# Optimization experiments

Hardware: AMD Instinct MI355X
Metric: run time of the kernel (lower is better)

Reference implementation:

```python
import jax, jax.numpy as jnp
import numpy as np

NPOINT = 1024
RADIUS = 0.2
NSAMPLE = 64
BN_EPS = 1e-5


def setup_inputs() -> dict:
    key = jax.random.key(0)
    ks = jax.random.split(key, 16)
    B, N = 8, 8192
    inp = {
        "xyz": jax.random.normal(ks[0], (B, 3, N), jnp.float32),
        "points": jax.random.normal(ks[1], (B, 3, N), jnp.float32),
        "seed_inds": jax.random.randint(ks[2], (B, N), 0, N),
    }
    chans = [6, 64, 64, 128]
    for i in range(3):
        cin, cout = chans[i], chans[i + 1]
        kk = jax.random.split(ks[3 + i], 3)
        inp[f"w{i}"] = jax.random.normal(kk[0], (cout, cin), jnp.float32) / np.sqrt(cin)
        inp[f"b{i}"] = jnp.zeros((cout,), jnp.float32)
        inp[f"g{i}"] = jnp.ones((cout,), jnp.float32)
        inp[f"be{i}"] = jnp.zeros((cout,), jnp.float32)
        inp[f"m{i}"] = jax.random.normal(kk[1], (cout,), jnp.float32) * 0.1
        inp[f"v{i}"] = jax.random.uniform(kk[2], (cout,), jnp.float32, 0.5, 1.5)
    return inp


def _fps(xyz, npoint):
    # xyz: [B, N, 3]. Deterministic start at index 0 (torch uses a random start).
    B, N, _ = xyz.shape

    def step(carry, _):
        dist, far = carry
        cent = jnp.take_along_axis(xyz, far[:, None, None], axis=1)  # [B,1,3]
        d = jnp.sum((xyz - cent) ** 2, -1)                           # [B,N]
        dist = jnp.minimum(dist, d)
        nxt = jnp.argmax(dist, -1)
        return (dist, nxt), far

    init = (jnp.full((B, N), 1e10, xyz.dtype), jnp.zeros((B,), jnp.int32))
    _, idxs = jax.lax.scan(step, init, None, length=npoint)
    return idxs.T  # [B, npoint]


def _sqdist(src, dst):
    # src [B,S,3], dst [B,N,3] -> [B,S,N]
    d = -2.0 * jnp.einsum("bsc,bnc->bsn", src, dst)
    d += jnp.sum(src ** 2, -1)[:, :, None]
    d += jnp.sum(dst ** 2, -1)[:, None, :]
    return d


def _gather(pts, idx):
    # pts [B,N,C], idx [B,S,K] -> [B,S,K,C]
    B, S, K = idx.shape
    flat = jnp.take_along_axis(pts, idx.reshape(B, S * K, 1), axis=1)
    return flat.reshape(B, S, K, pts.shape[-1])


def _forward(xyz, points, seed_inds, layers):
    xyz_t = xyz.transpose(0, 2, 1)      # [B,N,3]
    pts_t = points.transpose(0, 2, 1)   # [B,N,D]
    B, N, _ = xyz_t.shape

    fps_idx = _fps(xyz_t, NPOINT)                                   # [B,S]
    new_seed = jnp.take_along_axis(seed_inds, fps_idx.astype(seed_inds.dtype), axis=1)
    new_xyz = jnp.take_along_axis(xyz_t, fps_idx[:, :, None], axis=1)  # [B,S,3]

    # ball query via sort trick (same math as torch module)
    sq = _sqdist(new_xyz, xyz_t)                                    # [B,S,N]
    gi = jnp.where(sq > RADIUS ** 2, N, jnp.arange(N, dtype=jnp.int32)[None, None, :])
    gi = jnp.sort(gi, axis=-1)[:, :, :NSAMPLE]                      # [B,S,K]
    first = gi[:, :, :1]
    gi = jnp.where(gi == N, first, gi)

    gxyz = _gather(xyz_t, gi) - new_xyz[:, :, None, :]              # [B,S,K,3]
    gpts = _gather(pts_t, gi)                                       # [B,S,K,D]
    feat = jnp.concatenate([gxyz, gpts], -1)                        # [B,S,K,3+D]

    for (w, b, g, be, m, v) in layers:
        feat = jnp.einsum("bskc,oc->bsko", feat, w) + b             # 1x1 conv
        feat = (feat - m) * (g / jnp.sqrt(v + BN_EPS)) + be         # BN (inference)
        feat = jax.nn.relu(feat)

    new_points = jnp.max(feat, axis=2).transpose(0, 2, 1)           # [B,Cout,S]
    return new_xyz.transpose(0, 2, 1), new_points, new_seed


def reference(xyz, points, seed_inds,
              w0, b0, g0, be0, m0, v0,
              w1, b1, g1, be1, m1, v1,
              w2, b2, g2, be2, m2, v2):
    layers = [(w0, b0, g0, be0, m0, v0),
              (w1, b1, g1, be1, m1, v1),
              (w2, b2, g2, be2, m2, v2)]
    return _forward(xyz, points, seed_inds, layers)
```

## Files before the change

### kernel.cpp

```cpp
#include <hip/hip_runtime.h>

#define B_ 8
#define N_ 8192
#define S_ 1024
#define NS_ 64

typedef float v2f __attribute__((ext_vector_type(2)));
typedef unsigned long long u64;
typedef short bf16x8 __attribute__((ext_vector_type(8)));
typedef float f32x4 __attribute__((ext_vector_type(4)));

#define OUT0 0
#define OUT1 24576
#define OUT2 1073152

template <int CTRL>
static __device__ __forceinline__ float dpp_max_step(float v) {
    int o = __builtin_amdgcn_update_dpp(__float_as_int(v), __float_as_int(v),
                                        CTRL, 0xf, 0xf, false);
    return fmaxf(v, __int_as_float(o));
}
static __device__ __forceinline__ float wave_max_f32(float v) {
    v = dpp_max_step<0x111>(v);
    v = dpp_max_step<0x112>(v);
    v = dpp_max_step<0x114>(v);
    v = dpp_max_step<0x118>(v);
    v = dpp_max_step<0x142>(v);
    v = dpp_max_step<0x143>(v);
    return __int_as_float(__builtin_amdgcn_readlane(__float_as_int(v), 63));
}
template <int CTRL>
static __device__ __forceinline__ unsigned dpp_umin_step(unsigned v) {
    unsigned o = (unsigned)__builtin_amdgcn_update_dpp((int)v, (int)v,
                                                       CTRL, 0xf, 0xf, false);
    return v < o ? v : o;
}
static __device__ __forceinline__ unsigned wave_min_u32(unsigned v) {
    v = dpp_umin_step<0x111>(v);
    v = dpp_umin_step<0x112>(v);
    v = dpp_umin_step<0x114>(v);
    v = dpp_umin_step<0x118>(v);
    v = dpp_umin_step<0x142>(v);
    v = dpp_umin_step<0x143>(v);
    return (unsigned)__builtin_amdgcn_readlane((int)v, 63);
}

static __device__ __forceinline__ short f2bf(float f) {
    unsigned u = __float_as_uint(f);
    return (short)((u + 0x7FFFu + ((u >> 16) & 1u)) >> 16);
}

#define FPS_T 256
#define FPS_J 16

__global__ __launch_bounds__(FPS_T, 1) void fps_kernel(const float* __restrict__ xyz,
                                                       float* out) {
    const int b = blockIdx.x;
    const int t = threadIdx.x;
    const int lane = t & 63;
    const int wq = t >> 6;
    const float* X = xyz + b * 3 * N_;

    v2f px2[FPS_J], py2[FPS_J], pz2[FPS_J], dist2[FPS_J];
#pragma unroll
    for (int j = 0; j < FPS_J; ++j) {
        int n = t + 512 * j;
        px2[j] = (v2f){X[n], X[n + 256]};
        py2[j] = (v2f){X[N_ + n], X[N_ + n + 256]};
        pz2[j] = (v2f){X[2 * N_ + n], X[2 * N_ + n + 256]};
        dist2[j] = (v2f){1e10f, 1e10f};
    }

    __shared__ u64 slots[8];
    float* oseed = out + OUT2 + b * S_;

    int ci = 0;
    float c0 = X[0], c1 = X[N_], c2 = X[2 * N_];

    for (int step = 0; step < S_; ++step) {
        if (t == 0) oseed[step] = __int_as_float(ci);

        v2f mv = (v2f){-1.0f, -1.0f};
        {
#pragma clang fp contract(off)
            v2f c0v = (v2f){c0, c0};
            v2f c1v = (v2f){c1, c1};
            v2f c2v = (v2f){c2, c2};
#pragma unroll
            for (int j = 0; j < FPS_J; ++j) {
                v2f e0 = px2[j] - c0v;
                v2f e1 = py2[j] - c1v;
                v2f e2 = pz2[j] - c2v;
                v2f q0 = e0 * e0;
                v2f q1 = e1 * e1;
                v2f q2 = e2 * e2;
                v2f d  = (q0 + q1) + q2;
                v2f dm = __builtin_elementwise_min(dist2[j], d);
                dist2[j] = dm;
                mv = __builtin_elementwise_max(mv, dm);
            }
        }
        float m = fmaxf(mv.x, mv.y);
        float wmax = wave_max_f32(m);

        unsigned mask = 0u;
#pragma unroll
        for (int j = 0; j < FPS_J; ++j) {
            if (dist2[j].x == wmax) mask |= (1u << (2 * j));
            if (dist2[j].y == wmax) mask |= (1u << (2 * j + 1));
        }
        unsigned cand = 0xffffffffu;
        if (mask) {
            unsigned c = (unsigned)(__ffs(mask) - 1);
            cand = (unsigned)t | (c << 8);
        }
        unsigned widx = wave_min_u32(cand);

        if (lane == 63) {
            u64 key = ((u64)__float_as_uint(wmax) << 13) | (u64)(8191u - widx);
            slots[((step & 1) << 2) + wq] = key;
        }
        __syncthreads();

        const u64* sp = &slots[(step & 1) << 2];
        u64 k0 = sp[0], k1 = sp[1], k2 = sp[2], k3 = sp[3];
        u64 ka = (k0 > k1) ? k0 : k1;
        u64 kb = (k2 > k3) ? k2 : k3;
        u64 km = (ka > kb) ? ka : kb;
        ci = 8191 - (int)(km & 0x1fffull);

        int cu = __builtin_amdgcn_readfirstlane(ci);
        c0 = X[cu];
        c1 = X[N_ + cu];
        c2 = X[2 * N_ + cu];
    }
}

__global__ __launch_bounds__(256) void wconv_kernel(const float* __restrict__ w1,
                                                    const float* __restrict__ w2,
                                                    short* __restrict__ wbf) {
    int t = blockIdx.x * 256 + threadIdx.x;
    float v = (t < 4096) ? w1[t] : w2[t - 4096];
    wbf[t] = f2bf(v);
}

__global__ __launch_bounds__(256) void down_kernel(
    const float* __restrict__ xyz, const float* __restrict__ pts,
    const int* __restrict__ seed,
    const float* __restrict__ w0, const float* __restrict__ b0,
    const float* __restrict__ g0, const float* __restrict__ be0,
    const float* __restrict__ m0, const float* __restrict__ v0,
    const float* __restrict__ w1, const float* __restrict__ b1,
    const float* __restrict__ g1, const float* __restrict__ be1,
    const float* __restrict__ m1, const float* __restrict__ v1,
    const float* __restrict__ w2, const float* __restrict__ b2,
    const float* __restrict__ g2, const float* __restrict__ be2,
    const float* __restrict__ m2, const float* __restrict__ v2,
    float* out, const short* __restrict__ wbf) {
    const int sg = blockIdx.x;
    const int b = sg >> 10, s = sg & 1023;
    const int t = threadIdx.x;
    const int lane = t & 63;
    const int wq = __builtin_amdgcn_readfirstlane(t >> 6);
    const int ln = lane & 15;
    const int quad = (lane >> 4) & 3;

    __shared__ float f0[64 * 9];
    __shared__ short featA[64 * 72];
    __shared__ short featB[64 * 72];
    __shared__ float wmaxs[4 * 132];
    __shared__ float scs[256], ofs[256];
    __shared__ int cand[4 * 64];
    __shared__ int cnts[4];
    __shared__ int gis[64];

    const float* X = xyz + b * 3 * N_;

    int ci = __float_as_int(out[OUT2 + sg]) & 8191;
    float cx = X[ci], cy = X[N_ + ci], cz = X[2 * N_ + ci];

    {
        float sc, of;
        if (t < 64) {
            int c = t;
            sc = g0[c] / sqrtf(v0[c] + 1e-5f);
            of = (b0[c] - m0[c]) * sc + be0[c];
        } else if (t < 128) {
            int c = t - 64;
            sc = g1[c] / sqrtf(v1[c] + 1e-5f);
            of = (b1[c] - m1[c]) * sc + be1[c];
        } else {
            int c = t - 128;
            sc = g2[c] / sqrtf(v2[c] + 1e-5f);
            of = (b2[c] - m2[c]) * sc + be2[c];
        }
        scs[t] = sc;
        ofs[t] = of;
    }
    __syncthreads();

    if (t == 0) {
        out[OUT0 + (b * 3 + 0) * S_ + s] = cx;
        out[OUT0 + (b * 3 + 1) * S_ + s] = cy;
        out[OUT0 + (b * 3 + 2) * S_ + s] = cz;
        out[OUT2 + sg] = (float)seed[b * N_ + ci];
    }

    {
        int cnt = 0;
        const int wbase = wq << 11;
#pragma unroll 2
        for (int base = 0; base < 2048; base += 128) {
            int n0 = wbase + base + lane;
            int n1 = n0 + 64;
            float x0 = X[n0], y0 = X[N_ + n0], z0 = X[2 * N_ + n0];
            float x1 = X[n1], y1 = X[N_ + n1], z1 = X[2 * N_ + n1];
            float e0 = x0 - cx, e1 = y0 - cy, e2 = z0 - cz;
            float d0 = fmaf(e2, e2, fmaf(e1, e1, e0 * e0));
            float q0 = x1 - cx, q1 = y1 - cy, q2 = z1 - cz;
            float d1 = fmaf(q2, q2, fmaf(q1, q1, q0 * q0));

            u64 mask0 = __ballot(d0 <= 0.04f);
            if (mask0) {
                int pos = cnt + (int)__popcll(mask0 & ((1ull << lane) - 1ull));
                if ((d0 <= 0.04f) && pos < NS_) cand[(wq << 6) + pos] = n0;
                cnt += (int)__popcll(mask0);
            }
            u64 mask1 = __ballot(d1 <= 0.04f);
            if (mask1) {
                int pos = cnt + (int)__popcll(mask1 & ((1ull << lane) - 1ull));
                if ((d1 <= 0.04f) && pos < NS_) cand[(wq << 6) + pos] = n1;
                cnt += (int)__popcll(mask1);
            }
        }
        if (lane == 0) cnts[wq] = cnt;
    }
    __syncthreads();

    if (t < 64) {
        int k = t;
        int start = 0, sel = -1, firstv = -1;
#pragma unroll
        for (int w = 0; w < 4; ++w) {
            int cw = min(cnts[w], NS_);
            if (firstv < 0 && cw > 0) firstv = cand[(w << 6)];
            if (sel < 0 && k < start + cw) sel = cand[(w << 6) + (k - start)];
            start += cw;
        }
        if (sel < 0) sel = firstv;
        gis[t] = sel;
    }
    __syncthreads();

    if (t < 64) {
        int gidx = gis[t] & 8191;
        const float* P = pts + b * 3 * N_;
        f0[t * 9 + 0] = X[gidx] - cx;
        f0[t * 9 + 1] = X[N_ + gidx] - cy;
        f0[t * 9 + 2] = X[2 * N_ + gidx] - cz;
        f0[t * 9 + 3] = P[gidx];
        f0[t * 9 + 4] = P[N_ + gidx];
        f0[t * 9 + 5] = P[2 * N_ + gidx];
    }
    __syncthreads();

    {
        float in[6];
#pragma unroll
        for (int c = 0; c < 6; ++c) in[c] = f0[lane * 9 + c];
#pragma unroll 1
        for (int i = 0; i < 16; i += 4) {
            int o = wq * 16 + i;
            float a0 = 0.f, a1 = 0.f, a2 = 0.f, a3 = 0.f;
#pragma unroll
            for (int c = 0; c < 6; ++c) {
                float rc = in[c];
                a0 = fmaf(rc, w0[(o + 0) * 6 + c], a0);
                a1 = fmaf(rc, w0[(o + 1) * 6 + c], a1);
                a2 = fmaf(rc, w0[(o + 2) * 6 + c], a2);
                a3 = fmaf(rc, w0[(o + 3) * 6 + c], a3);
            }
            featA[lane * 72 + o + 0] = f2bf(fmaxf(fmaf(a0, scs[o + 0], ofs[o + 0]), 0.f));
            featA[lane * 72 + o + 1] = f2bf(fmaxf(fmaf(a1, scs[o + 1], ofs[o + 1]), 0.f));
            featA[lane * 72 + o + 2] = f2bf(fmaxf(fmaf(a2, scs[o + 2], ofs[o + 2]), 0.f));
            featA[lane * 72 + o + 3] = f2bf(fmaxf(fmaf(a3, scs[o + 3], ofs[o + 3]), 0.f));
        }
    }
    __syncthreads();

    const int arow = 16 * wq + ln;
    const bool usebf = (wbf != nullptr);

    {
        bf16x8 a1f[2];
#pragma unroll
        for (int ks = 0; ks < 2; ++ks)
            a1f[ks] = *(const bf16x8*)&featA[arow * 72 + ks * 32 + quad * 8];

#pragma unroll
        for (int nt = 0; nt < 4; ++nt) {
            f32x4 acc = {0.f, 0.f, 0.f, 0.f};
#pragma unroll
            for (int ks = 0; ks < 2; ++ks) {
                int off = (nt * 16 + ln) * 64 + ks * 32 + quad * 8;
                bf16x8 bf;
                if (usebf) {
                    bf = *(const bf16x8*)&wbf[off];
                } else {
                    const float* wr = w1 + off;
                    float4 p = *(const float4*)wr;
                    float4 q = *(const float4*)(wr + 4);
                    bf = (bf16x8){f2bf(p.x), f2bf(p.y), f2bf(p.z), f2bf(p.w),
                                  f2bf(q.x), f2bf(q.y), f2bf(q.z), f2bf(q.w)};
                }
                acc = __builtin_amdgcn_mfma_f32_16x16x32_bf16(a1f[ks], bf, acc, 0, 0, 0);
            }
            int o = nt * 16 + ln;
            float sc = scs[64 + o], of = ofs[64 + o];
#pragma unroll
            for (int reg = 0; reg < 4; ++reg) {
                float y = fmaxf(fmaf(acc[reg], sc, of), 0.f);
                featB[(16 * wq + quad * 4 + reg) * 72 + o] = f2bf(y);
            }
        }
    }

    {
        bf16x8 a2f[2];
#pragma unroll
        for (int ks = 0; ks < 2; ++ks)
            a2f[ks] = *(const bf16x8*)&featB[arow * 72 + ks * 32 + quad * 8];

#pragma unroll
        for (int nt = 0; nt < 8; ++nt) {
            f32x4 acc = {0.f, 0.f, 0.f, 0.f};
#pragma unroll
            for (int ks = 0; ks < 2; ++ks) {
                int off = (nt * 16 + ln) * 64 + ks * 32 + quad * 8;
                bf16x8 bf;
                if (usebf) {
                    bf = *(const bf16x8*)&wbf[4096 + off];
                } else {
                    const float* wr = w2 + off;
                    float4 p = *(const float4*)wr;
                    float4 q = *(const float4*)(wr + 4);
                    bf = (bf16x8){f2bf(p.x), f2bf(p.y), f2bf(p.z), f2bf(p.w),
                                  f2bf(q.x), f2bf(q.y), f2bf(q.z), f2bf(q.w)};
                }
                acc = __builtin_amdgcn_mfma_f32_16x16x32_bf16(a2f[ks], bf, acc, 0, 0, 0);
            }
            int o = nt * 16 + ln;
            float sc = scs[128 + o], of = ofs[128 + o];
            float m = -1.f;
#pragma unroll
            for (int reg = 0; reg < 4; ++reg) {
                float y = fmaxf(fmaf(acc[reg], sc, of), 0.f);
                m = fmaxf(m, y);
            }
            m = fmaxf(m, __shfl_xor(m, 16, 64));
            m = fmaxf(m, __shfl_xor(m, 32, 64));
            if (lane < 16) wmaxs[wq * 132 + o] = m;
        }
    }
    __syncthreads();

    if (t < 128) {
        float m = fmaxf(fmaxf(wmaxs[0 * 132 + t], wmaxs[1 * 132 + t]),
                        fmaxf(wmaxs[2 * 132 + t], wmaxs[3 * 132 + t]));
        out[OUT1 + (b * 128 + t) * S_ + s] = m;
    }
}

extern "C" void kernel_launch(void* const* d_in, const int* in_sizes, int n_in,
                              void* d_out, int out_size, void* d_ws, size_t ws_size,
                              hipStream_t stream) {
    const float* xyz  = (const float*)d_in[0];
    const float* pts  = (const float*)d_in[1];
    const int*   seed = (const int*)d_in[2];
    const float* w0 = (const float*)d_in[3];
    const float* b0 = (const float*)d_in[4];
    const float* g0 = (const float*)d_in[5];
    const float* be0 = (const float*)d_in[6];
    const float* m0 = (const float*)d_in[7];
    const float* v0 = (const float*)d_in[8];
    const float* w1 = (const float*)d_in[9];
    const float* b1 = (const float*)d_in[10];
    const float* g1 = (const float*)d_in[11];
    const float* be1 = (const float*)d_in[12];
    const float* m1 = (const float*)d_in[13];
    const float* v1 = (const float*)d_in[14];
    const float* w2 = (const float*)d_in[15];
    const float* b2 = (const float*)d_in[16];
    const float* g2 = (const float*)d_in[17];
    const float* be2 = (const float*)d_in[18];
    const float* m2 = (const float*)d_in[19];
    const float* v2 = (const float*)d_in[20];
    float* out = (float*)d_out;

    short* wbf = nullptr;
    if (ws_size >= 12288 * sizeof(short)) {
        wbf = (short*)d_ws;
        wconv_kernel<<<dim3(48), dim3(256), 0, stream>>>(w1, w2, wbf);
    }

    fps_kernel<<<dim3(B_), dim3(FPS_T), 0, stream>>>(xyz, out);
    down_kernel<<<dim3(B_ * S_), dim3(256), 0, stream>>>(xyz, pts, seed,
        w0, b0, g0, be0, m0, v0,
        w1, b1, g1, be1, m1, v1,
        w2, b2, g2, be2, m2, v2,
        out, wbf);
}
```

Before: 1.256 ms.

## Split farthest point sampling per batch across four blocks with global-memory flag exchange

Farthest point sampling previously ran one 256-thread block per batch. It now runs four blocks per batch, 32 in total, and each wave keeps 512 points in registers. Waves exchange their per-step argmax keys through tagged 64-bit slots in workspace memory, using release stores and spin loads, then reduce them with DPP. This spreads the serial 1024-step loop over more compute units so each step does less work. In exchange it adds cross-block synchronisation latency per step and depends on all 32 blocks being resident at once; the spin guard bounds a deadlock but could yield wrong indices.

```diff
diff --git a/kernel.cpp b/kernel.cpp
--- a/kernel.cpp
+++ b/kernel.cpp
@@ -13,6 +13,11 @@
 #define OUT0 0
 #define OUT1 24576
 #define OUT2 1073152
+
+#define WS_WBF_BYTES   24576
+#define WS_FLAGS_OFF   24576
+#define WS_FLAGS_BYTES 2048
+#define WS_MULTI_NEED  (WS_FLAGS_OFF + WS_FLAGS_BYTES)
 
 template <int CTRL>
 static __device__ __forceinline__ float dpp_max_step(float v) {
@@ -44,10 +49,124 @@
     v = dpp_umin_step<0x143>(v);
     return (unsigned)__builtin_amdgcn_readlane((int)v, 63);
 }
+template <int CTRL>
+static __device__ __forceinline__ u64 dpp_umax64_step(u64 v) {
+    int lo = (int)(unsigned)v;
+    int hi = (int)(unsigned)(v >> 32);
+    int olo = __builtin_amdgcn_update_dpp(lo, lo, CTRL, 0xf, 0xf, false);
+    int ohi = __builtin_amdgcn_update_dpp(hi, hi, CTRL, 0xf, 0xf, false);
+    u64 o = ((u64)(unsigned)ohi << 32) | (u64)(unsigned)olo;
+    return (v > o) ? v : o;
+}
 
 static __device__ __forceinline__ short f2bf(float f) {
     unsigned u = __float_as_uint(f);
     return (short)((u + 0x7FFFu + ((u >> 16) & 1u)) >> 16);
+}
+
+__global__ __launch_bounds__(256, 1) void fps_multi_kernel(const float* __restrict__ xyz,
+                                                           float* out,
+                                                           u64* __restrict__ F) {
+    const int bid = blockIdx.x;
+    const int b = bid & 7;
+    const int rr = bid >> 3;
+    const int t = threadIdx.x;
+    const int lane = t & 63;
+    const int w16 = (rr << 2) | (t >> 6);
+    const float* X = xyz + b * 3 * N_;
+    const int base = w16 << 9;
+
+    v2f px2[4], py2[4], pz2[4], dist2[4];
+#pragma unroll
+    for (int j = 0; j < 4; ++j) {
+        int n = base + lane + 128 * j;
+        px2[j] = (v2f){X[n], X[n + 64]};
+        py2[j] = (v2f){X[N_ + n], X[N_ + n + 64]};
+        pz2[j] = (v2f){X[2 * N_ + n], X[2 * N_ + n + 64]};
+        dist2[j] = (v2f){1e10f, 1e10f};
+    }
+
+    float* oseed = out + OUT2 + b * S_;
+    u64* Fb = F + (b << 5);
+
+    int ci = 0;
+    float c0 = X[0], c1 = X[N_], c2 = X[2 * N_];
+
+    for (int step = 0; step < S_; ++step) {
+        if (rr == 0 && t == 0) oseed[step] = __int_as_float(ci);
+
+        v2f mv = (v2f){-1.0f, -1.0f};
+        {
+#pragma clang fp contract(off)
+            v2f c0v = (v2f){c0, c0};
+            v2f c1v = (v2f){c1, c1};
+            v2f c2v = (v2f){c2, c2};
+#pragma unroll
+            for (int j = 0; j < 4; ++j) {
+                v2f e0 = px2[j] - c0v;
+                v2f e1 = py2[j] - c1v;
+                v2f e2 = pz2[j] - c2v;
+                v2f q0 = e0 * e0;
+                v2f q1 = e1 * e1;
+                v2f q2 = e2 * e2;
+                v2f d  = (q0 + q1) + q2;
+                v2f dm = __builtin_elementwise_min(dist2[j], d);
+                dist2[j] = dm;
+                mv = __builtin_elementwise_max(mv, dm);
+            }
+        }
+        float m = fmaxf(mv.x, mv.y);
+        float wmax = wave_max_f32(m);
+
+        unsigned mask = 0u;
+#pragma unroll
+        for (int j = 0; j < 4; ++j) {
+            if (dist2[j].x == wmax) mask |= (1u << (2 * j));
+            if (dist2[j].y == wmax) mask |= (1u << (2 * j + 1));
+        }
+        unsigned cand = 0xffffffffu;
+        if (mask) {
+            unsigned c = (unsigned)(__ffs(mask) - 1);
+            cand = (unsigned)lane | (c << 6);
+        }
+        unsigned widx = wave_min_u32(cand);
+        unsigned gidx = (unsigned)base + widx;
+
+        const u64 tag = (u64)(step + 1);
+        const u64 okey = (tag << 45) |
+                         ((u64)__float_as_uint(wmax) << 13) |
+                         (u64)(8191u - gidx);
+        u64* slot = Fb + (((step + 1) & 1) << 4);
+
+        if (lane == 0)
+            __hip_atomic_store(&slot[w16], okey, __ATOMIC_RELEASE,
+                               __HIP_MEMORY_SCOPE_AGENT);
+
+        u64 kk = okey;
+        bool need = (lane < 15);
+        const int rw = (w16 + 1 + lane) & 15;
+        int guard = 0;
+        while (__any((int)need)) {
+            if (need) {
+                u64 v = __hip_atomic_load(&slot[rw], __ATOMIC_RELAXED,
+                                          __HIP_MEMORY_SCOPE_AGENT);
+                if ((v >> 45) == tag) { kk = v; need = false; }
+            }
+            if (++guard > (1 << 20)) break;
+        }
+
+        kk = dpp_umax64_step<0x111>(kk);
+        kk = dpp_umax64_step<0x112>(kk);
+        kk = dpp_umax64_step<0x114>(kk);
+        kk = dpp_umax64_step<0x118>(kk);
+        unsigned klo = (unsigned)__builtin_amdgcn_readlane((int)(unsigned)kk, 15);
+        ci = 8191 - (int)(klo & 0x1fffu);
+
+        int cu = __builtin_amdgcn_readfirstlane(ci);
+        c0 = X[cu];
+        c1 = X[N_ + cu];
+        c2 = X[2 * N_ + cu];
+    }
 }
 
 #define FPS_T 256
@@ -138,10 +257,15 @@
 
 __global__ __launch_bounds__(256) void wconv_kernel(const float* __restrict__ w1,
                                                     const float* __restrict__ w2,
-                                                    short* __restrict__ wbf) {
+                                                    short* __restrict__ wbf,
+                                                    u64* __restrict__ F) {
     int t = blockIdx.x * 256 + threadIdx.x;
-    float v = (t < 4096) ? w1[t] : w2[t - 4096];
-    wbf[t] = f2bf(v);
+    if (F != nullptr && blockIdx.x == 0)
+        F[threadIdx.x] = 0ull;
+    if (t < 12288) {
+        float v = (t < 4096) ? w1[t] : w2[t - 4096];
+        wbf[t] = f2bf(v);
+    }
 }
 
 __global__ __launch_bounds__(256) void down_kernel(
@@ -398,12 +522,15 @@
     float* out = (float*)d_out;
 
     short* wbf = nullptr;
-    if (ws_size >= 12288 * sizeof(short)) {
-        wbf = (short*)d_ws;
-        wconv_kernel<<<dim3(48), dim3(256), 0, stream>>>(w1, w2, wbf);
-    }
-
-    fps_kernel<<<dim3(B_), dim3(FPS_T), 0, stream>>>(xyz, out);
+    u64* F = nullptr;
+    if (ws_size >= 12288 * sizeof(short)) wbf = (short*)d_ws;
+    if (ws_size >= (size_t)WS_MULTI_NEED) F = (u64*)((char*)d_ws + WS_FLAGS_OFF);
+
+    if (wbf) wconv_kernel<<<dim3(48), dim3(256), 0, stream>>>(w1, w2, wbf, F);
+
+    if (F) fps_multi_kernel<<<dim3(32), dim3(256), 0, stream>>>(xyz, out, F);
+    else   fps_kernel<<<dim3(B_), dim3(FPS_T), 0, stream>>>(xyz, out);
+
     down_kernel<<<dim3(B_ * S_), dim3(256), 0, stream>>>(xyz, pts, seed,
         w0, b0, g0, be0, m0, v0,
         w1, b1, g1, be1, m1, v1,
```

Result: slower. 2.287 ms (+82.0%).

## Replace FPS barrier with tagged LDS spin handshake and fused 64-bit key reduction

Applied to the files above, without the earlier changes.

The farthest-point-sampling loop drops the per-step __syncthreads. Each wave instead publishes a step-tagged 64-bit key (tag, distance, index) with an atomic release store, then spins on LDS until all four wave slots carry the current tag. The separate float max and index min wave reductions become a single 64-bit DPP max. Seed indices are buffered in LDS and written to global memory once at the end rather than every step. The aim is to cut barrier and reduction latency on the serial 1024-step critical path, at the cost of spin-wait polling, a guard-bounded loop, and 64-bit DPP ops (two per step).

```diff
diff --git a/kernel.cpp b/kernel.cpp
--- a/kernel.cpp
+++ b/kernel.cpp
@@ -15,34 +15,22 @@
 #define OUT2 1073152
 
 template <int CTRL>
-static __device__ __forceinline__ float dpp_max_step(float v) {
-    int o = __builtin_amdgcn_update_dpp(__float_as_int(v), __float_as_int(v),
-                                        CTRL, 0xf, 0xf, false);
-    return fmaxf(v, __int_as_float(o));
-}
-static __device__ __forceinline__ float wave_max_f32(float v) {
-    v = dpp_max_step<0x111>(v);
-    v = dpp_max_step<0x112>(v);
-    v = dpp_max_step<0x114>(v);
-    v = dpp_max_step<0x118>(v);
-    v = dpp_max_step<0x142>(v);
-    v = dpp_max_step<0x143>(v);
-    return __int_as_float(__builtin_amdgcn_readlane(__float_as_int(v), 63));
-}
-template <int CTRL>
-static __device__ __forceinline__ unsigned dpp_umin_step(unsigned v) {
-    unsigned o = (unsigned)__builtin_amdgcn_update_dpp((int)v, (int)v,
-                                                       CTRL, 0xf, 0xf, false);
-    return v < o ? v : o;
-}
-static __device__ __forceinline__ unsigned wave_min_u32(unsigned v) {
-    v = dpp_umin_step<0x111>(v);
-    v = dpp_umin_step<0x112>(v);
-    v = dpp_umin_step<0x114>(v);
-    v = dpp_umin_step<0x118>(v);
-    v = dpp_umin_step<0x142>(v);
-    v = dpp_umin_step<0x143>(v);
-    return (unsigned)__builtin_amdgcn_readlane((int)v, 63);
+static __device__ __forceinline__ u64 dpp_umax64_step(u64 v) {
+    int lo = (int)(unsigned)v;
+    int hi = (int)(unsigned)(v >> 32);
+    int olo = __builtin_amdgcn_update_dpp(lo, lo, CTRL, 0xf, 0xf, false);
+    int ohi = __builtin_amdgcn_update_dpp(hi, hi, CTRL, 0xf, 0xf, false);
+    u64 o = ((u64)(unsigned)ohi << 32) | (u64)(unsigned)olo;
+    return (v > o) ? v : o;
+}
+static __device__ __forceinline__ u64 wave_max_u64(u64 v) {
+    v = dpp_umax64_step<0x111>(v);
+    v = dpp_umax64_step<0x112>(v);
+    v = dpp_umax64_step<0x114>(v);
+    v = dpp_umax64_step<0x118>(v);
+    v = dpp_umax64_step<0x142>(v);
+    v = dpp_umax64_step<0x143>(v);
+    return v;
 }
 
 static __device__ __forceinline__ short f2bf(float f) {
@@ -58,7 +46,6 @@
     const int b = blockIdx.x;
     const int t = threadIdx.x;
     const int lane = t & 63;
-    const int wq = t >> 6;
     const float* X = xyz + b * 3 * N_;
 
     v2f px2[FPS_J], py2[FPS_J], pz2[FPS_J], dist2[FPS_J];
@@ -72,13 +59,15 @@
     }
 
     __shared__ u64 slots[8];
-    float* oseed = out + OUT2 + b * S_;
+    __shared__ float seedL[S_];
+    if (t < 8) slots[t] = 0ull;
+    __syncthreads();
 
     int ci = 0;
     float c0 = X[0], c1 = X[N_], c2 = X[2 * N_];
 
     for (int step = 0; step < S_; ++step) {
-        if (t == 0) oseed[step] = __int_as_float(ci);
+        if (t == 0) seedL[step] = __int_as_float(ci);
 
         v2f mv = (v2f){-1.0f, -1.0f};
         {
@@ -101,39 +90,56 @@
             }
         }
         float m = fmaxf(mv.x, mv.y);
-        float wmax = wave_max_f32(m);
 
         unsigned mask = 0u;
 #pragma unroll
         for (int j = 0; j < FPS_J; ++j) {
-            if (dist2[j].x == wmax) mask |= (1u << (2 * j));
-            if (dist2[j].y == wmax) mask |= (1u << (2 * j + 1));
-        }
-        unsigned cand = 0xffffffffu;
-        if (mask) {
-            unsigned c = (unsigned)(__ffs(mask) - 1);
-            cand = (unsigned)t | (c << 8);
-        }
-        unsigned widx = wave_min_u32(cand);
-
-        if (lane == 63) {
-            u64 key = ((u64)__float_as_uint(wmax) << 13) | (u64)(8191u - widx);
-            slots[((step & 1) << 2) + wq] = key;
-        }
-        __syncthreads();
-
-        const u64* sp = &slots[(step & 1) << 2];
-        u64 k0 = sp[0], k1 = sp[1], k2 = sp[2], k3 = sp[3];
-        u64 ka = (k0 > k1) ? k0 : k1;
-        u64 kb = (k2 > k3) ? k2 : k3;
-        u64 km = (ka > kb) ? ka : kb;
-        ci = 8191 - (int)(km & 0x1fffull);
+            if (dist2[j].x == m) mask |= (1u << (2 * j));
+            if (dist2[j].y == m) mask |= (1u << (2 * j + 1));
+        }
+        unsigned c = (unsigned)(__ffs(mask) - 1);
+        unsigned n = (unsigned)t | (c << 8);
+
+        const u64 tag = (u64)(step + 1);
+        u64 key = (tag << 45) |
+                  ((u64)__float_as_uint(m) << 13) |
+                  (u64)(8191u - n);
+
+        key = wave_max_u64(key);
+
+        u64* sp = &slots[((step + 1) & 1) << 2];
+        if (lane == 63)
+            __hip_atomic_store(&sp[t >> 6], key, __ATOMIC_RELEASE,
+                               __HIP_MEMORY_SCOPE_WORKGROUP);
+
+        u64 kk = 0ull;
+        bool need = (lane < 4);
+        int guard = 0;
+        while (__any((int)need)) {
+            if (need) {
+                u64 v = __hip_atomic_load(&sp[lane], __ATOMIC_RELAXED,
+                                          __HIP_MEMORY_SCOPE_WORKGROUP);
+                if ((v >> 45) == tag) { kk = v; need = false; }
+            }
+            if (++guard > (1 << 20)) break;
+        }
+
+        kk = dpp_umax64_step<0x111>(kk);
+        kk = dpp_umax64_step<0x112>(kk);
+        unsigned klo = (unsigned)__builtin_amdgcn_readlane((int)(unsigned)kk, 3);
+        ci = 8191 - (int)(klo & 0x1fffu);
 
         int cu = __builtin_amdgcn_readfirstlane(ci);
         c0 = X[cu];
         c1 = X[N_ + cu];
         c2 = X[2 * N_ + cu];
     }
+
+    __syncthreads();
+    float* oseed = out + OUT2 + b * S_;
+#pragma unroll
+    for (int k = 0; k < 4; ++k)
+        oseed[t + 256 * k] = seedL[t + 256 * k];
 }
 
 __global__ __launch_bounds__(256) void wconv_kernel(const float* __restrict__ w1,
```

Result: slower. 1.362 ms (+8.4%).
